# Kernel optimization log

Measured on AMD Instinct MI355X. Metric: run time of the kernel, lower is better.

The kernel has to match this reference:

```python
import jax, jax.numpy as jnp
import numpy as np

B, T, H = 4, 2048, 1024
NH = 16
HD = H // NH  # 64
FF = 4 * H


def setup_inputs() -> dict:
    key = jax.random.key(0)
    ks = jax.random.split(key, 11)
    s = 0.02
    return {
        "x": jax.random.normal(ks[0], (B, T, H), dtype=jnp.float32),
        "Wq": jax.random.normal(ks[1], (H, H), dtype=jnp.float32) * s,
        "bq": jnp.zeros((H,), dtype=jnp.float32),
        "Wk": jax.random.normal(ks[2], (H, H), dtype=jnp.float32) * s,
        "bk": jnp.zeros((H,), dtype=jnp.float32),
        "Wv": jax.random.normal(ks[3], (H, H), dtype=jnp.float32) * s,
        "bv": jnp.zeros((H,), dtype=jnp.float32),
        "W1": jax.random.normal(ks[4], (H, FF), dtype=jnp.float32) * s,
        "b1": jnp.zeros((FF,), dtype=jnp.float32),
        "W2": jax.random.normal(ks[5], (FF, H), dtype=jnp.float32) * s,
        "b2": jnp.zeros((H,), dtype=jnp.float32),
    }


def _block(x, Wq, bq, Wk, bk, Wv, bv, W1, b1, W2, b2):
    b, t, h = x.shape
    # multi-head masked self-attention; NOTE: scale = full h_dim ** 0.5 (as in source)
    q = (x @ Wq + bq).reshape(b, t, NH, HD).transpose(0, 2, 1, 3)  # [B,nH,T,HD]
    k = (x @ Wk + bk).reshape(b, t, NH, HD).transpose(0, 2, 1, 3)
    v = (x @ Wv + bv).reshape(b, t, NH, HD).transpose(0, 2, 1, 3)
    att = jnp.einsum("bnqd,bnkd->bnqk", q, k) / (h ** 0.5)  # [B,nH,T,T]
    causal = jnp.tril(jnp.ones((t, t), dtype=bool))
    att = jnp.where(causal, att, -jnp.inf)
    w = jax.nn.softmax(att, axis=-1)
    attn_out = jnp.einsum("bnqk,bnkd->bnqd", w, v).transpose(0, 2, 1, 3).reshape(b, t, h)
    x = x + attn_out
    # MLP (dropout p=0 -> identity)
    mlp = jax.nn.gelu(x @ W1 + b1) @ W2 + b2
    return x + mlp


def reference(x, Wq, bq, Wk, bk, Wv, bv, W1, b1, W2, b2):
    return _block(x, Wq, bq, Wk, bk, Wv, bv, W1, b1, W2, b2)
```

## Files before the change

### kernel.cpp

```cpp
#include <hip/hip_runtime.h>
#include <cstdint>
#include <cstddef>

typedef unsigned short u16;
typedef __attribute__((ext_vector_type(8))) __bf16 bf16x8;
typedef __attribute__((ext_vector_type(4))) __bf16 bf16x4;
typedef __attribute__((ext_vector_type(4))) float f32x4;
typedef __attribute__((ext_vector_type(4))) u16 u16x4;

#define MFMA(a, b, c) __builtin_amdgcn_mfma_f32_16x16x32_bf16((a), (b), (c), 0, 0, 0)

__device__ __forceinline__ u16 f2b(float f) {
  union { float f; unsigned u; } v;
  v.f = f;
  unsigned r = v.u + 0x7fffu + ((v.u >> 16) & 1u);
  return (u16)(r >> 16);
}

__device__ __forceinline__ void gld16(const void* g, void* l) {
  __builtin_amdgcn_global_load_lds(
      (__attribute__((address_space(1))) void*)(void*)(g),
      (__attribute__((address_space(3))) void*)(l), 16, 0, 0);
}

__device__ __forceinline__ size_t qk_off(int t, int hd) {
  return (size_t)((((t >> 4) * 2 + (hd >> 5)) * 512)
                  + ((((hd >> 3) & 3) * 16 + (t & 15)) * 8) + (hd & 7));
}
__device__ __forceinline__ size_t v_off(int t, int hd) {
  int kk = ((t & 15) << 2) | ((t >> 4) & 3);
  return (size_t)(((t >> 6) * 4096)
                  + (((hd >> 4) * 2 + (kk >> 5)) * 512)
                  + ((((kk >> 3) & 3) * 16 + (hd & 15)) * 8) + (kk & 7));
}

__global__ void xconv(const float* __restrict__ in, u16* __restrict__ out, int n) {
  int i = (blockIdx.x * blockDim.x + threadIdx.x) * 4;
  if (i >= n) return;
  float4 v = *(const float4*)(in + i);
  u16x4 o;
  o[0] = f2b(v.x); o[1] = f2b(v.y); o[2] = f2b(v.z); o[3] = f2b(v.w);
  *(u16x4*)(out + i) = o;
}

__global__ void wtrans(const float* __restrict__ W, u16* __restrict__ Wt, int Kd, int Nd) {
  __shared__ float tile[32][33];
  int n0 = blockIdx.x * 32, k0 = blockIdx.y * 32;
  int tx = threadIdx.x, ty = threadIdx.y;
#pragma unroll
  for (int i = 0; i < 4; i++)
    tile[ty + i * 8][tx] = W[(size_t)(k0 + ty + i * 8) * Nd + n0 + tx];
  __syncthreads();
#pragma unroll
  for (int i = 0; i < 4; i++)
    Wt[(size_t)(n0 + ty + i * 8) * Kd + k0 + tx] = f2b(tile[tx][ty + i * 8]);
}

template <int MODE>
__global__ __launch_bounds__(256) void gemm_bt(
    const u16* __restrict__ A, const u16* __restrict__ Bt,
    const float* __restrict__ b0, const float* __restrict__ b1,
    const float* __restrict__ b2, void* __restrict__ outp,
    const float* __restrict__ resid, int N, int K, float scale) {
  __shared__ __attribute__((aligned(16))) u16 As[128 * 32];
  __shared__ __attribute__((aligned(16))) u16 Bs[128 * 32];
  const int tid = threadIdx.x;
  const int wid = tid >> 6, lane = tid & 63;
  const int g = lane >> 4, r = lane & 15;
  const int bm = blockIdx.y, bn = blockIdx.x;
  const int wrow = (wid >> 1) * 64, wcol = (wid & 1) * 64;

  const f32x4 zero4 = {0.f, 0.f, 0.f, 0.f};
  f32x4 acc[4][4];
#pragma unroll
  for (int i = 0; i < 4; i++)
#pragma unroll
    for (int j = 0; j < 4; j++) acc[i][j] = zero4;

  const size_t aBase = (size_t)bm * 128 * K;
  const size_t bBase = (size_t)bn * 128 * K;

  for (int k0 = 0; k0 < K; k0 += 32) {
    __syncthreads();
#pragma unroll
    for (int i = 0; i < 2; i++) {
      int c = i * 256 + tid;
      int row = c >> 2, ko = (c & 3) * 8;
      gld16(A + aBase + (size_t)row * K + k0 + ko, As + c * 8);
      gld16(Bt + bBase + (size_t)row * K + k0 + ko, Bs + c * 8);
    }
    __syncthreads();
    bf16x8 af[4], bfr[4];
#pragma unroll
    for (int t = 0; t < 4; t++) {
      af[t] = *(const bf16x8*)&As[(wrow + t * 16 + r) * 32 + g * 8];
      bfr[t] = *(const bf16x8*)&Bs[(wcol + t * 16 + r) * 32 + g * 8];
    }
#pragma unroll
    for (int mt = 0; mt < 4; mt++)
#pragma unroll
      for (int nt = 0; nt < 4; nt++) acc[mt][nt] = MFMA(af[mt], bfr[nt], acc[mt][nt]);
  }

#pragma unroll
  for (int mt = 0; mt < 4; mt++) {
#pragma unroll
    for (int nt = 0; nt < 4; nt++) {
      int col = bn * 128 + wcol + nt * 16 + r;
      float bv;
      if (MODE == 4) {
        int sec = col >> 10, hcol = col & 1023;
        bv = (sec == 0) ? b0[hcol] : (sec == 1) ? b1[hcol] : b2[hcol];
      } else {
        bv = b0[col];
      }
#pragma unroll
      for (int rr = 0; rr < 4; rr++) {
        int row = bm * 128 + wrow + mt * 16 + g * 4 + rr;
        float v = acc[mt][nt][rr] + bv;
        if (MODE == 2) {
          float u = 0.7978845608028654f * (v + 0.044715f * v * v * v);
          float th = 1.0f - 2.0f / (1.0f + __expf(2.0f * u));
          ((u16*)outp)[(size_t)row * N + col] = f2b(0.5f * v * (1.0f + th));
        } else if (MODE == 3) {
          ((float*)outp)[(size_t)row * N + col] = v + resid[(size_t)row * N + col];
        } else if (MODE == 4) {
          int sec = col >> 10, hcol = col & 1023;
          int head = hcol >> 6, hd = hcol & 63;
          int bb = row >> 11, t = row & 2047;
          size_t hbase = ((size_t)bb * 16 + head) * 131072;
          u16* qout = (u16*)outp;
          if (sec == 0) {
            qout[hbase + qk_off(t, hd)] = f2b(v * scale);
          } else if (sec == 1) {
            (qout + 8388608)[hbase + qk_off(t, hd)] = f2b(v);
          } else {
            (qout + 16777216)[hbase + v_off(t, hd)] = f2b(v);
          }
        }
      }
    }
  }
}

__global__ __launch_bounds__(256) void attn_kernel(
    const u16* __restrict__ Q, const u16* __restrict__ Kc,
    const u16* __restrict__ Vt, const float* __restrict__ x,
    float* __restrict__ x1, u16* __restrict__ xb1) {
  const int bh = blockIdx.x & 63;
  const int slot = blockIdx.x >> 6;
  const int tid = threadIdx.x;
  const int wid = tid >> 6, lane = tid & 63;
  const int g = lane >> 4, c = lane & 15;
  const u16* Qh = Q + (size_t)bh * 131072;
  const u16* Kh = Kc + (size_t)bh * 131072;
  const u16* Vh = Vt + (size_t)bh * 131072;
  const int b = bh >> 4, head = bh & 15;

  __shared__ __attribute__((aligned(16))) u16 Ks[8192];
  __shared__ __attribute__((aligned(16))) u16 Vs[8192];
  __shared__ __attribute__((aligned(16))) u16 P[4][32][72];

  bf16x8 ones;
#pragma unroll
  for (int i = 0; i < 8; i++) ones[i] = (__bf16)1.0f;

  const f32x4 zero4 = {0.f, 0.f, 0.f, 0.f};

  for (int phase = 0; phase < 2; ++phase) {
    const int bt = phase ? (15 - slot) : slot;
    const int q0b = bt * 128;
    const int q0 = q0b + wid * 32;
    const int kendw = q0 + 32;
    const int nkt = bt + 1;

    bf16x8 qf[2][2];
#pragma unroll
    for (int mt = 0; mt < 2; mt++)
#pragma unroll
      for (int h = 0; h < 2; h++)
        qf[mt][h] = *(const bf16x8*)&Qh[(((q0 >> 4) + mt) * 2 + h) * 512 + lane * 8];

    f32x4 o[2][4];
    f32x4 lac[2];
#pragma unroll
    for (int mt = 0; mt < 2; mt++) {
      lac[mt] = zero4;
#pragma unroll
      for (int i = 0; i < 4; i++) o[mt][i] = zero4;
    }

    for (int kt = 0; kt < nkt; ++kt) {
      const int k0 = kt * 128;
#pragma unroll
      for (int r2 = 0; r2 < 4; r2++) {
        int idx = (r2 * 256 + tid) * 8;
        gld16(Kh + (size_t)k0 * 64 + idx, Ks + idx);
        gld16(Vh + (size_t)k0 * 64 + idx, Vs + idx);
      }
      __syncthreads();

#pragma unroll
      for (int s2 = 0; s2 < 2; ++s2) {
        const int k0s = k0 + s2 * 64;
        if (k0s < kendw) {
          bf16x8 kf[4][2], vf[4][2];
#pragma unroll
          for (int nt = 0; nt < 4; nt++)
#pragma unroll
            for (int h = 0; h < 2; h++) {
              kf[nt][h] = *(const bf16x8*)&Ks[s2 * 4096 + (nt * 2 + h) * 512 + lane * 8];
              vf[nt][h] = *(const bf16x8*)&Vs[s2 * 4096 + (nt * 2 + h) * 512 + lane * 8];
            }

          f32x4 sv[2][4];
#pragma unroll
          for (int mt = 0; mt < 2; mt++)
#pragma unroll
            for (int nt = 0; nt < 4; nt++) sv[mt][nt] = zero4;
#pragma unroll
          for (int nt = 0; nt < 4; nt++)
#pragma unroll
            for (int mt = 0; mt < 2; mt++) {
              sv[mt][nt] = MFMA(qf[mt][0], kf[nt][0], sv[mt][nt]);
              sv[mt][nt] = MFMA(qf[mt][1], kf[nt][1], sv[mt][nt]);
            }

          if (k0s + 64 > q0) {
#pragma unroll
            for (int mt = 0; mt < 2; mt++)
#pragma unroll
              for (int rr = 0; rr < 4; rr++) {
                int q = q0 + mt * 16 + g * 4 + rr;
#pragma unroll
                for (int nt = 0; nt < 4; nt++)
                  if (k0s + nt * 16 + c > q) sv[mt][nt][rr] = -1e30f;
              }
          }

#pragma unroll
          for (int mt = 0; mt < 2; mt++)
#pragma unroll
            for (int rr = 0; rr < 4; rr++) {
              union { u16x4 u; bf16x4 h; } pw;
#pragma unroll
              for (int nt = 0; nt < 4; nt++)
                pw.h[nt] = (__bf16)__builtin_amdgcn_exp2f(sv[mt][nt][rr]);
              *(u16x4*)&P[wid][mt * 16 + g * 4 + rr][4 * c] = pw.u;
            }

          asm volatile("s_waitcnt lgkmcnt(0)" ::: "memory");

#pragma unroll
          for (int mt = 0; mt < 2; mt++) {
            bf16x8 pf0 = *(const bf16x8*)&P[wid][mt * 16 + c][g * 8];
            bf16x8 pf1 = *(const bf16x8*)&P[wid][mt * 16 + c][32 + g * 8];
            lac[mt] = MFMA(pf0, ones, lac[mt]);
            lac[mt] = MFMA(pf1, ones, lac[mt]);
#pragma unroll
            for (int ot = 0; ot < 4; ot++) {
              f32x4 oo = MFMA(pf0, vf[ot][0], o[mt][ot]);
              o[mt][ot] = MFMA(pf1, vf[ot][1], oo);
            }
          }
        }
      }
      __syncthreads();
    }

    float inv[2][4];
#pragma unroll
    for (int mt = 0; mt < 2; mt++)
#pragma unroll
      for (int rr = 0; rr < 4; rr++) inv[mt][rr] = 1.0f / lac[mt][rr];
#pragma unroll
    for (int mt = 0; mt < 2; mt++)
#pragma unroll
      for (int ot = 0; ot < 4; ot++)
#pragma unroll
        for (int rr = 0; rr < 4; rr++) {
          int t = q0 + mt * 16 + g * 4 + rr;
          int hd = ot * 16 + c;
          size_t xi = ((size_t)b * 2048 + t) * 1024 + head * 64 + hd;
          float v = x[xi] + o[mt][ot][rr] * inv[mt][rr];
          x1[xi] = v;
          xb1[xi] = f2b(v);
        }
  }
}

extern "C" void kernel_launch(void* const* d_in, const int* in_sizes, int n_in,
                              void* d_out, int out_size, void* d_ws, size_t ws_size,
                              hipStream_t stream) {
  (void)in_sizes; (void)n_in; (void)out_size; (void)ws_size;
  const float* x = (const float*)d_in[0];
  const float* Wq = (const float*)d_in[1];
  const float* bq = (const float*)d_in[2];
  const float* Wk = (const float*)d_in[3];
  const float* bk = (const float*)d_in[4];
  const float* Wv = (const float*)d_in[5];
  const float* bv = (const float*)d_in[6];
  const float* W1 = (const float*)d_in[7];
  const float* b1 = (const float*)d_in[8];
  const float* W2 = (const float*)d_in[9];
  const float* b2 = (const float*)d_in[10];

  char* ws = (char*)d_ws;
  size_t off = 0;
  auto alloc = [&](size_t bytes) {
    char* p = ws + off;
    off += (bytes + 255) & ~(size_t)255;
    return p;
  };
  u16* xb    = (u16*)alloc(8192ull * 1024 * 2);
  u16* Wqkvt = (u16*)alloc(3072ull * 1024 * 2);
  u16* W1t   = (u16*)alloc(4096ull * 1024 * 2);
  u16* W2t   = (u16*)alloc(1024ull * 4096 * 2);
  u16* Qb    = (u16*)alloc(3ull * 8192 * 1024 * 2);
  float* x1  = (float*)alloc(8192ull * 1024 * 4);
  u16* hb    = (u16*)alloc(8192ull * 4096 * 2);
  u16* xb1   = xb;
  u16* Kb    = Qb + 8388608;
  u16* Vtb   = Qb + 16777216;

  const float qscale = 1.4426950408889634f / 32.0f;

  xconv<<<dim3(8192), dim3(256), 0, stream>>>(x, xb, 8192 * 1024);
  wtrans<<<dim3(32, 32), dim3(32, 8), 0, stream>>>(Wq, Wqkvt, 1024, 1024);
  wtrans<<<dim3(32, 32), dim3(32, 8), 0, stream>>>(Wk, Wqkvt + 1024 * 1024, 1024, 1024);
  wtrans<<<dim3(32, 32), dim3(32, 8), 0, stream>>>(Wv, Wqkvt + 2048 * 1024, 1024, 1024);
  wtrans<<<dim3(128, 32), dim3(32, 8), 0, stream>>>(W1, W1t, 1024, 4096);
  wtrans<<<dim3(32, 128), dim3(32, 8), 0, stream>>>(W2, W2t, 4096, 1024);
  gemm_bt<4><<<dim3(24, 64), dim3(256), 0, stream>>>(
      xb, Wqkvt, bq, bk, bv, Qb, nullptr, 3072, 1024, qscale);
  attn_kernel<<<dim3(512), dim3(256), 0, stream>>>(Qb, Kb, Vtb, x, x1, xb1);
  gemm_bt<2><<<dim3(32, 64), dim3(256), 0, stream>>>(
      xb1, W1t, b1, nullptr, nullptr, hb, nullptr, 4096, 1024, 1.0f);
  gemm_bt<3><<<dim3(8, 64), dim3(256), 0, stream>>>(
      hb, W2t, b2, nullptr, nullptr, d_out, x1, 1024, 4096, 1.0f);
}
```

Measured before the change: 483.0 us.

## Deepen GEMM K-tile with swizzled LDS, fuse weight transposes, cheaper GELU

The GEMM now stages 64-wide K tiles with an XOR swizzle on the LDS layout to avoid bank conflicts and halve the number of sync rounds. An 8-wave variant is added and used for the W2 projection. The five weight-transpose launches become one kernel. GELU is rewritten as the tanh approximation in sigmoid form using exp2, and bf16 conversion uses the native cast. These cut launch overhead, LDS conflicts and ALU work, at the cost of more LDS per block and possible occupancy changes.

```diff
diff --git a/kernel.cpp b/kernel.cpp
--- a/kernel.cpp
+++ b/kernel.cpp
@@ -11,10 +11,9 @@
 #define MFMA(a, b, c) __builtin_amdgcn_mfma_f32_16x16x32_bf16((a), (b), (c), 0, 0, 0)
 
 __device__ __forceinline__ u16 f2b(float f) {
-  union { float f; unsigned u; } v;
-  v.f = f;
-  unsigned r = v.u + 0x7fffu + ((v.u >> 16) & 1u);
-  return (u16)(r >> 16);
+  union { __bf16 h; u16 u; } v;
+  v.h = (__bf16)f;
+  return v.u;
 }
 
 __device__ __forceinline__ void gld16(const void* g, void* l) {
@@ -43,9 +42,27 @@
   *(u16x4*)(out + i) = o;
 }
 
-__global__ void wtrans(const float* __restrict__ W, u16* __restrict__ Wt, int Kd, int Nd) {
+__global__ void wtrans_all(const float* __restrict__ Wq, const float* __restrict__ Wk,
+                           const float* __restrict__ Wv, const float* __restrict__ W1,
+                           const float* __restrict__ W2, u16* __restrict__ Wqkvt,
+                           u16* __restrict__ W1t, u16* __restrict__ W2t) {
   __shared__ float tile[32][33];
-  int n0 = blockIdx.x * 32, k0 = blockIdx.y * 32;
+  int blk = blockIdx.x;
+  const float* W;
+  u16* Wt;
+  int Kd, Nd, nx;
+  if (blk < 3072) {
+    int s = blk >> 10;
+    blk &= 1023;
+    W = (s == 0) ? Wq : (s == 1) ? Wk : Wv;
+    Wt = Wqkvt + (size_t)s * 1048576;
+    Kd = 1024; Nd = 1024; nx = 32;
+  } else if (blk < 7168) {
+    blk -= 3072; W = W1; Wt = W1t; Kd = 1024; Nd = 4096; nx = 128;
+  } else {
+    blk -= 7168; W = W2; Wt = W2t; Kd = 4096; Nd = 1024; nx = 32;
+  }
+  int n0 = (blk % nx) * 32, k0 = (blk / nx) * 32;
   int tx = threadIdx.x, ty = threadIdx.y;
 #pragma unroll
   for (int i = 0; i < 4; i++)
@@ -56,56 +73,71 @@
     Wt[(size_t)(n0 + ty + i * 8) * Kd + k0 + tx] = f2b(tile[tx][ty + i * 8]);
 }
 
-template <int MODE>
-__global__ __launch_bounds__(256) void gemm_bt(
+template <int MODE, int NW>
+__global__ __launch_bounds__(NW * 64) void gemm_bt(
     const u16* __restrict__ A, const u16* __restrict__ Bt,
     const float* __restrict__ b0, const float* __restrict__ b1,
     const float* __restrict__ b2, void* __restrict__ outp,
     const float* __restrict__ resid, int N, int K, float scale) {
-  __shared__ __attribute__((aligned(16))) u16 As[128 * 32];
-  __shared__ __attribute__((aligned(16))) u16 Bs[128 * 32];
+  constexpr int NT = NW * 64;
+  constexpr int NTILE = (NW == 4) ? 4 : 2;
+  __shared__ __attribute__((aligned(16))) u16 As[128 * 64];
+  __shared__ __attribute__((aligned(16))) u16 Bs[128 * 64];
   const int tid = threadIdx.x;
   const int wid = tid >> 6, lane = tid & 63;
   const int g = lane >> 4, r = lane & 15;
   const int bm = blockIdx.y, bn = blockIdx.x;
-  const int wrow = (wid >> 1) * 64, wcol = (wid & 1) * 64;
+  const int wrow = (NW == 4) ? (wid >> 1) * 64 : (wid >> 2) * 64;
+  const int wcol = (NW == 4) ? (wid & 1) * 64 : (wid & 3) * 32;
 
   const f32x4 zero4 = {0.f, 0.f, 0.f, 0.f};
-  f32x4 acc[4][4];
+  f32x4 acc[4][NTILE];
 #pragma unroll
   for (int i = 0; i < 4; i++)
 #pragma unroll
-    for (int j = 0; j < 4; j++) acc[i][j] = zero4;
+    for (int j = 0; j < NTILE; j++) acc[i][j] = zero4;
 
   const size_t aBase = (size_t)bm * 128 * K;
   const size_t bBase = (size_t)bn * 128 * K;
-
-  for (int k0 = 0; k0 < K; k0 += 32) {
+  const int ko0 = ((0 * 4 + g) ^ (r & 7)) * 8;
+  const int ko1 = ((1 * 4 + g) ^ (r & 7)) * 8;
+
+  for (int k0 = 0; k0 < K; k0 += 64) {
     __syncthreads();
 #pragma unroll
-    for (int i = 0; i < 2; i++) {
-      int c = i * 256 + tid;
-      int row = c >> 2, ko = (c & 3) * 8;
-      gld16(A + aBase + (size_t)row * K + k0 + ko, As + c * 8);
-      gld16(Bt + bBase + (size_t)row * K + k0 + ko, Bs + c * 8);
+    for (int i = 0; i < 2048 / NT; i++) {
+      const int c0 = i * NT;
+      const int cc = (c0 + tid) & 1023;
+      const int row = cc >> 3;
+      const int js = ((cc & 7) ^ (row & 7)) * 8;
+      if (c0 < 1024)
+        gld16(A + aBase + (size_t)row * K + k0 + js, As + cc * 8);
+      else
+        gld16(Bt + bBase + (size_t)row * K + k0 + js, Bs + cc * 8);
     }
     __syncthreads();
-    bf16x8 af[4], bfr[4];
-#pragma unroll
-    for (int t = 0; t < 4; t++) {
-      af[t] = *(const bf16x8*)&As[(wrow + t * 16 + r) * 32 + g * 8];
-      bfr[t] = *(const bf16x8*)&Bs[(wcol + t * 16 + r) * 32 + g * 8];
-    }
-#pragma unroll
-    for (int mt = 0; mt < 4; mt++)
-#pragma unroll
-      for (int nt = 0; nt < 4; nt++) acc[mt][nt] = MFMA(af[mt], bfr[nt], acc[mt][nt]);
+#pragma unroll
+    for (int kh = 0; kh < 2; kh++) {
+      const int ko = kh ? ko1 : ko0;
+      bf16x8 af[4], bfr[NTILE];
+#pragma unroll
+      for (int t = 0; t < 4; t++)
+        af[t] = *(const bf16x8*)&As[(wrow + t * 16 + r) * 64 + ko];
+#pragma unroll
+      for (int t = 0; t < NTILE; t++)
+        bfr[t] = *(const bf16x8*)&Bs[(wcol + t * 16 + r) * 64 + ko];
+#pragma unroll
+      for (int mt = 0; mt < 4; mt++)
+#pragma unroll
+        for (int nt = 0; nt < NTILE; nt++)
+          acc[mt][nt] = MFMA(af[mt], bfr[nt], acc[mt][nt]);
+    }
   }
 
 #pragma unroll
   for (int mt = 0; mt < 4; mt++) {
 #pragma unroll
-    for (int nt = 0; nt < 4; nt++) {
+    for (int nt = 0; nt < NTILE; nt++) {
       int col = bn * 128 + wcol + nt * 16 + r;
       float bv;
       if (MODE == 4) {
@@ -119,9 +151,12 @@
         int row = bm * 128 + wrow + mt * 16 + g * 4 + rr;
         float v = acc[mt][nt][rr] + bv;
         if (MODE == 2) {
-          float u = 0.7978845608028654f * (v + 0.044715f * v * v * v);
-          float th = 1.0f - 2.0f / (1.0f + __expf(2.0f * u));
-          ((u16*)outp)[(size_t)row * N + col] = f2b(0.5f * v * (1.0f + th));
+          const float c1 = -2.3025850929940457f;
+          const float c2 = c1 * 0.044715f;
+          float t2 = v * v;
+          float z = v * (c1 + c2 * t2);
+          float sg = 1.0f / (1.0f + __builtin_amdgcn_exp2f(z));
+          ((u16*)outp)[(size_t)row * N + col] = f2b(v * sg);
         } else if (MODE == 3) {
           ((float*)outp)[(size_t)row * N + col] = v + resid[(size_t)row * N + col];
         } else if (MODE == 4) {
@@ -326,16 +361,13 @@
   const float qscale = 1.4426950408889634f / 32.0f;
 
   xconv<<<dim3(8192), dim3(256), 0, stream>>>(x, xb, 8192 * 1024);
-  wtrans<<<dim3(32, 32), dim3(32, 8), 0, stream>>>(Wq, Wqkvt, 1024, 1024);
-  wtrans<<<dim3(32, 32), dim3(32, 8), 0, stream>>>(Wk, Wqkvt + 1024 * 1024, 1024, 1024);
-  wtrans<<<dim3(32, 32), dim3(32, 8), 0, stream>>>(Wv, Wqkvt + 2048 * 1024, 1024, 1024);
-  wtrans<<<dim3(128, 32), dim3(32, 8), 0, stream>>>(W1, W1t, 1024, 4096);
-  wtrans<<<dim3(32, 128), dim3(32, 8), 0, stream>>>(W2, W2t, 4096, 1024);
-  gemm_bt<4><<<dim3(24, 64), dim3(256), 0, stream>>>(
+  wtrans_all<<<dim3(11264), dim3(32, 8), 0, stream>>>(
+      Wq, Wk, Wv, W1, W2, Wqkvt, W1t, W2t);
+  gemm_bt<4, 4><<<dim3(24, 64), dim3(256), 0, stream>>>(
       xb, Wqkvt, bq, bk, bv, Qb, nullptr, 3072, 1024, qscale);
   attn_kernel<<<dim3(512), dim3(256), 0, stream>>>(Qb, Kb, Vtb, x, x1, xb1);
-  gemm_bt<2><<<dim3(32, 64), dim3(256), 0, stream>>>(
+  gemm_bt<2, 4><<<dim3(32, 64), dim3(256), 0, stream>>>(
       xb1, W1t, b1, nullptr, nullptr, hb, nullptr, 4096, 1024, 1.0f);
-  gemm_bt<3><<<dim3(8, 64), dim3(256), 0, stream>>>(
+  gemm_bt<3, 8><<<dim3(8, 64), dim3(512), 0, stream>>>(
       hb, W2t, b2, nullptr, nullptr, d_out, x1, 1024, 4096, 1.0f);
 }
```

Result: faster. 449.8 us (-6.9%).
